# Kernel tuning notes

Hardware: AMD Instinct MI355X
Metric: run time of the kernel (lower is better)

Reference implementation:

```python
import jax, jax.numpy as jnp
import numpy as np

# problem constants (from config / init_kwargs)
OBJ = 1024        # object_size
D = 256           # diffraction_size == probe_size (pad = 0)
P = 256           # probe_size
S = 8             # num_slices
B = 256           # batch of scan indices
NSCAN = 4096      # number of scan positions
PX = 0.1          # pixel_size (Angstrom)
LAM = 0.0197      # wavelength (Angstrom, ~300 kV)
CONV = 0.025      # convergence angle (rad)
DZ = 2.0          # slice thickness (Angstrom)


def _freq_grids():
    f = jnp.fft.fftfreq(D, d=PX).astype(jnp.float32)
    kx, ky = jnp.meshgrid(f, f, indexing='ij')
    return kx, ky


def _probe(defocus, Cs, astig_mag, astig_angle, aperture_smooth):
    kx, ky = _freq_grids()
    k = jnp.sqrt(kx ** 2 + ky ** 2)
    k_angle = jnp.arctan2(ky, kx)
    chi = (np.pi * LAM * defocus * k ** 2
           + 0.5 * np.pi * LAM ** 3 * (Cs * 1e6) * k ** 4
           + np.pi * LAM * astig_mag * k ** 2 * jnp.cos(2.0 * (k_angle - astig_angle)))
    k_max = CONV / LAM
    smooth = jnp.abs(aperture_smooth) + 0.01
    aperture = jax.nn.sigmoid((k_max - k) / (k_max * smooth))
    probe_k = aperture.astype(jnp.complex64) * jnp.exp(1j * chi.astype(jnp.complex64))
    probe_real = jnp.fft.ifftshift(jnp.fft.ifft2(probe_k))
    probe_real = probe_real / jnp.sqrt(jnp.sum(jnp.abs(probe_real) ** 2))
    # crop(P) with P == D and c == h is the identity slice [0:D, 0:D]
    return probe_real


def _propagator():
    kx, ky = _freq_grids()
    k2 = kx ** 2 + ky ** 2
    return jnp.exp(1j * (np.pi * LAM * DZ * k2).astype(jnp.complex64))


def setup_inputs() -> dict:
    key = jax.random.key(0)
    k1, k2, k3, k4 = jax.random.split(key, 4)
    slice_amp = jnp.ones((S, OBJ, OBJ), dtype=jnp.float32) \
        + 0.05 * jax.random.normal(k1, (S, OBJ, OBJ), dtype=jnp.float32)
    slice_phase = 0.1 * jax.random.normal(k2, (S, OBJ, OBJ), dtype=jnp.float32)
    scan_positions = jax.random.randint(k3, (NSCAN, 2), 0, OBJ - P, dtype=jnp.int32)
    indices = jax.random.randint(k4, (B,), 0, NSCAN, dtype=jnp.int32)
    return {
        'slice_amp': slice_amp,
        'slice_phase': slice_phase,
        'defocus': jnp.float32(50.0),
        'Cs': jnp.float32(0.5),
        'astig_mag': jnp.float32(10.0),
        'astig_angle': jnp.float32(0.0),
        'aperture_smooth': jnp.float32(0.1),
        'scan_positions': scan_positions,
        'indices': indices,
    }


def reference(slice_amp, slice_phase, defocus, Cs, astig_mag, astig_angle,
              aperture_smooth, scan_positions, indices):
    probe = _probe(defocus, Cs, astig_mag, astig_angle, aperture_smooth)  # [D,D] c64
    H = _propagator()                                                      # [D,D] c64
    pos = scan_positions[indices]                                          # [B,2] (y,x)

    def gather_patch(t, yx):
        return jax.lax.dynamic_slice(t, (yx[0], yx[1]), (P, P))

    wave = jnp.broadcast_to(probe[None, :, :], (B, P, P))  # [B,P,P] c64
    for s in range(S):  # small fixed slice recurrence
        t = slice_amp[s].astype(jnp.complex64) * jnp.exp(1j * slice_phase[s].astype(jnp.complex64))
        patches = jax.vmap(gather_patch, in_axes=(None, 0))(t, pos)  # [B,P,P]
        exit_wave = wave * patches                      # pad = 0 since P == D
        wave = jnp.fft.ifft2(jnp.fft.fft2(exit_wave) * H)
    psi = jnp.fft.fft2(wave)                            # [B,D,D] complex64
    return psi
```

## Files before the change

kernel.cpp:

```cpp
#include <hip/hip_runtime.h>
#include <hip/hip_fp16.h>
#include <math.h>

typedef unsigned short u16;
typedef unsigned int   u32;

__device__ __forceinline__ bool is_f64(const void* amp){
  u32 u = ((const u32*)amp)[1];
  return ((u >> 20) & 0xFFF) >= 0x3FB;
}
__device__ __forceinline__ bool is_i64(const void* spos){
  const u32* p = (const u32*)spos;
  return (p[1] | p[3] | p[5]) == 0;
}
__device__ __forceinline__ float ldf(const void* p, size_t i, bool f64){
  return f64 ? (float)((const double*)p)[i] : ((const float*)p)[i];
}
__device__ __forceinline__ double lds_scalar(const void* p, bool f64){
  return f64 ? ((const double*)p)[0] : (double)((const float*)p)[0];
}
__device__ __forceinline__ int ldi(const void* p, size_t i, bool i64){
  return i64 ? (int)((const long long*)p)[i] : ((const int*)p)[i];
}

__device__ __forceinline__ u16 f2bf(float f){
  u32 u = __float_as_uint(f);
  u32 r = 0x7fffu + ((u >> 16) & 1u);
  return (u16)((u + r) >> 16);
}
__device__ __forceinline__ void stout(void* p, size_t i, float2 v){
  ((u32*)p)[i] = (u32)f2bf(v.y) | ((u32)f2bf(v.x) << 16);
}

template<int H>
__device__ __forceinline__ float2 ld_state(const void* p, size_t i){
  if (H){
    __half2 h = ((const __half2*)p)[i];
    return __half22float2(h);
  }
  return ((const float2*)p)[i];
}
template<int H>
__device__ __forceinline__ void st_state(void* p, size_t i, float2 v){
  if (H) ((__half2*)p)[i] = __floats2half2_rn(v.x, v.y);
  else   ((float2*)p)[i] = v;
}

__device__ __forceinline__ float2 cadd(float2 a, float2 b){ return make_float2(a.x+b.x, a.y+b.y); }
__device__ __forceinline__ float2 csub(float2 a, float2 b){ return make_float2(a.x-b.x, a.y-b.y); }
__device__ __forceinline__ float2 cmul(float2 a, float2 b){ return make_float2(a.x*b.x - a.y*b.y, a.x*b.y + a.y*b.x); }
__device__ __forceinline__ float2 cmulc(float2 a, float2 b){ return make_float2(a.x*b.x + a.y*b.y, a.y*b.x - a.x*b.y); }
__device__ __forceinline__ float2 cscale(float2 a, float s){ return make_float2(a.x*s, a.y*s); }

template<int SGN>
__device__ __forceinline__ void fft4(float2& a, float2& b, float2& c, float2& d){
  float2 apc = cadd(a,c), amc = csub(a,c);
  float2 bpd = cadd(b,d), bmd = csub(b,d);
  float2 jb = (SGN < 0) ? make_float2(bmd.y, -bmd.x) : make_float2(-bmd.y, bmd.x);
  a = cadd(apc, bpd);
  b = cadd(amc, jb);
  c = csub(apc, bpd);
  d = csub(amc, jb);
}
template<int SGN>
__device__ __forceinline__ float2 twc(float2 z, float re, float im){
  float i2 = (SGN < 0) ? im : -im;
  return make_float2(z.x*re - z.y*i2, z.x*i2 + z.y*re);
}
template<int SGN>
__device__ __forceinline__ void fft16(float2 v[16]){
  float2 h[16];
#pragma unroll
  for (int n1=0;n1<4;n1++){
    float2 a=v[n1], b=v[n1+4], c=v[n1+8], d=v[n1+12];
    fft4<SGN>(a,b,c,d);
    h[n1*4+0]=a; h[n1*4+1]=b; h[n1*4+2]=c; h[n1*4+3]=d;
  }
  const float C1=0.92387953251f, S1=0.38268343236f, C2=0.70710678119f;
  h[5]  = twc<SGN>(h[5],  C1,-S1);
  h[6]  = twc<SGN>(h[6],  C2,-C2);
  h[7]  = twc<SGN>(h[7],  S1,-C1);
  h[9]  = twc<SGN>(h[9],  C2,-C2);
  h[10] = twc<SGN>(h[10], 0.f,-1.f);
  h[11] = twc<SGN>(h[11],-C2,-C2);
  h[13] = twc<SGN>(h[13], S1,-C1);
  h[14] = twc<SGN>(h[14],-C2,-C2);
  h[15] = twc<SGN>(h[15],-C1, S1);
#pragma unroll
  for (int q=0;q<4;q++){
    float2 a=h[q], b=h[4+q], c=h[8+q], d=h[12+q];
    fft4<SGN>(a,b,c,d);
    v[q]=a; v[q+4]=b; v[q+8]=c; v[q+12]=d;
  }
}

__device__ __forceinline__ void make_tw(float2 tw[15], int t){
  float s0, c0;
  sincosf(0.0245436926f * (float)t, &s0, &c0);
  float2 w1 = make_float2(c0, -s0);
  tw[0] = w1;
#pragma unroll
  for (int q=1;q<15;q++) tw[q] = cmul(tw[q-1], w1);
}

template<int SGN, int BARRIER>
__device__ __forceinline__ void fft256(float2 v[16], float* Tr, float* Ti, int g, int t,
                                       const float2 tw[15]){
  fft16<SGN>(v);
#pragma unroll
  for (int q=1;q<16;q++){
    v[q] = (SGN < 0) ? cmul(v[q], tw[q-1]) : cmulc(v[q], tw[q-1]);
  }
  int base = g*257;
  if (BARRIER) __syncthreads();
#pragma unroll
  for (int k1=0;k1<16;k1++){
    int o = base + t*16 + (k1^t);
    Tr[o] = v[k1].x; Ti[o] = v[k1].y;
  }
  if (BARRIER) __syncthreads();
#pragma unroll
  for (int n1=0;n1<16;n1++){
    int o = base + n1*16 + (t^n1);
    v[n1] = make_float2(Tr[o], Ti[o]);
  }
  fft16<SGN>(v);
  if (SGN > 0){
#pragma unroll
    for (int q=0;q<16;q++) v[q] = cscale(v[q], 1.f/256.f);
  }
}

__device__ __forceinline__ float ffreq(int i){ return (float)(i < 128 ? i : i - 256) * 0.0390625f; }

#define LDS_F 4112
#define KMAX  1.26903553299f
#define PHCONST 0.123778191f


__global__ void __launch_bounds__(256) probe_rowsF(const void* defocus, const void* Cs,
                                                   const void* astig_mag, const void* astig_angle,
                                                   const void* ap_smooth, const void* ampflag,
                                                   float2* tmp){
  __shared__ float Tr[LDS_F], Ti[LDS_F];
  bool f64 = is_f64(ampflag);
  int tid = threadIdx.x, g = tid>>4, t = tid&15;
  int r = blockIdx.x*16 + g;
  double df = lds_scalar(defocus, f64), cs = lds_scalar(Cs, f64);
  double am = lds_scalar(astig_mag, f64), aa = lds_scalar(astig_angle, f64);
  float sm = fabsf((float)lds_scalar(ap_smooth, f64)) + 0.01f;
  const double LAMd = 0.0197;
  float kxv = ffreq(r);
  float2 v[16];
#pragma unroll
  for (int j=0;j<16;j++){
    int c = t + 16*j;
    float kyv = ffreq(c);
    double k2 = (double)kxv*kxv + (double)kyv*kyv;
    float k  = sqrtf((float)k2);
    double ang = atan2((double)kyv, (double)kxv);
    double chi = M_PI*LAMd*df*k2
               + 0.5*M_PI*LAMd*LAMd*LAMd*(cs*1e6)*k2*k2
               + M_PI*LAMd*am*k2*cos(2.0*(ang - aa));
    float ap = 1.f/(1.f + expf(-(KMAX - k)/(KMAX*sm)));
    double sc = sin(chi), cc = cos(chi);
    v[j] = make_float2(ap*(float)cc, ap*(float)sc);
  }
  float2 tw[15]; make_tw(tw, t);
  fft256<1,0>(v, Tr, Ti, g, t, tw);
#pragma unroll
  for (int j=0;j<16;j++) tmp[(r<<8) + t + 16*j] = v[j];
}

__global__ void __launch_bounds__(256) probe_colsF(const float2* tmp, float2* probe_out,
                                                   const void* ap_smooth, const void* ampflag){
  __shared__ float Tr[LDS_F], Ti[LDS_F];
  bool f64 = is_f64(ampflag);
  int tid = threadIdx.x, xl = tid&15, t = tid>>4;
  int cx = blockIdx.x*16 + xl;
  float sm = fabsf((float)lds_scalar(ap_smooth, f64)) + 0.01f;
  float S = 0.f;
  for (int i = tid; i < 65536; i += 256){
    float kx = ffreq(i>>8), ky = ffreq(i&255);
    float k = sqrtf(kx*kx + ky*ky);
    float ap = 1.f/(1.f + expf(-(KMAX - k)/(KMAX*sm)));
    S += ap*ap;
  }
#pragma unroll
  for (int off=32; off>0; off>>=1) S += __shfl_down(S, off);
  if ((tid&63)==0) Tr[tid>>6] = S;
  __syncthreads();
  float scale = 256.f * rsqrtf(Tr[0]+Tr[1]+Tr[2]+Tr[3]);
  float2 v[16];
#pragma unroll
  for (int j=0;j<16;j++) v[j] = tmp[((t+16*j)<<8) + cx];
  float2 tw[15]; make_tw(tw, t);
  fft256<1,1>(v, Tr, Ti, xl, t, tw);
  int csh = (cx + 128) & 255;
#pragma unroll
  for (int j=0;j<16;j++){
    int y = t + 16*j;
    probe_out[(((y+128)&255)<<8) + csh] = cscale(v[j], scale);
  }
}

__global__ void __launch_bounds__(256) build_ttabF(const void* amp, const void* phase,
                                                   __half2* ttab){
  bool f64 = is_f64(amp);
  int tid = threadIdx.x;
#pragma unroll
  for (int k=0;k<4;k++){
    size_t i = (size_t)blockIdx.x*1024 + tid + 256*k;
    float A = ldf(amp, i, f64);
    float P = ldf(phase, i, f64);
    float sp, cp; sincosf(P, &sp, &cp);
    ttab[i] = __floats2half2_rn(A*cp, A*sp);
  }
}

template<int H>
__global__ void __launch_bounds__(256) row_passT(const void* amp, const void* phase,
                                                 const void* spos, const void* sidx,
                                                 void* state, const float2* probe,
                                                 const __half2* ttab, int s, int first,
                                                 int use_tt){
  __shared__ float Tr[LDS_F], Ti[LDS_F];
  bool f64 = is_f64(amp);
  bool i64 = is_i64(spos);
  int tid = threadIdx.x, g = tid>>4, t = tid&15;
  int b = blockIdx.y;
  int y = blockIdx.x*16 + g;
  int n = ldi(sidx, b, i64);
  int py = ldi(spos, 2*(size_t)n, i64), px = ldi(spos, 2*(size_t)n+1, i64);
  size_t rowbase = ((size_t)s<<20) + (size_t)(py+y)*1024 + px;
  float2 tv[16];
  if (use_tt){
#pragma unroll
    for (int j=0;j<16;j++) tv[j] = __half22float2(ttab[rowbase + t + 16*j]);
  } else {
#pragma unroll
    for (int j=0;j<16;j++){
      int x = t + 16*j;
      float A = ldf(amp,   rowbase + x, f64);
      float P = ldf(phase, rowbase + x, f64);
      float sp, cp; sincosf(P, &sp, &cp);
      tv[j] = make_float2(A*cp, A*sp);
    }
  }
  size_t ib = (size_t)b << 16;
  float2 tw[15]; make_tw(tw, t);
  float2 v[16];
  if (first){
#pragma unroll
    for (int j=0;j<16;j++) v[j] = probe[(y<<8) + t + 16*j];
  } else {
#pragma unroll
    for (int j=0;j<16;j++) v[j] = ld_state<H>(state, ib + (y<<8) + t + 16*j);
    fft256<1,0>(v, Tr, Ti, g, t, tw);
  }
#pragma unroll
  for (int j=0;j<16;j++) v[j] = cmul(v[j], tv[j]);
  fft256<-1,0>(v, Tr, Ti, g, t, tw);
#pragma unroll
  for (int j=0;j<16;j++) st_state<H>(state, ib + (y<<8) + t + 16*j, v[j]);
}

template<int H>
__global__ void __launch_bounds__(256) col_passT(void* state){
  __shared__ float Tr[LDS_F], Ti[LDS_F];
  __shared__ float2 h1[256];
  int tid = threadIdx.x, xl = tid&15, t = tid>>4;
  int b = blockIdx.y;
  int cx = blockIdx.x*16 + xl;
  size_t ib = (size_t)b << 16;
  {
    float kk = ffreq(tid);
    float a = PHCONST * kk * kk;
    float sa, ca; sincosf(a, &sa, &ca);
    h1[tid] = make_float2(ca, sa);
  }
  float2 tw[15]; make_tw(tw, t);
  float2 v[16];
#pragma unroll
  for (int j=0;j<16;j++) v[j] = ld_state<H>(state, ib + ((t+16*j)<<8) + cx);
  fft256<-1,1>(v, Tr, Ti, xl, t, tw);
  float2 hx = h1[cx & 255];
#pragma unroll
  for (int j=0;j<16;j++) v[j] = cmul(v[j], cmul(h1[t + 16*j], hx));
  fft256<1,1>(v, Tr, Ti, xl, t, tw);
#pragma unroll
  for (int j=0;j<16;j++) st_state<H>(state, ib + ((t+16*j)<<8) + cx, v[j]);
}

template<int H>
__global__ void __launch_bounds__(256) col_finT(void* state, void* outp){
  __shared__ float Tr[LDS_F], Ti[LDS_F];
  __shared__ float2 h1[256];
  int tid = threadIdx.x, xl = tid&15, t = tid>>4;
  int b = blockIdx.y;
  int cx = blockIdx.x*16 + xl;
  size_t ib = (size_t)b << 16;
  {
    float kk = ffreq(tid);
    float a = PHCONST * kk * kk;
    float sa, ca; sincosf(a, &sa, &ca);
    h1[tid] = make_float2(ca, sa);
  }
  float2 tw[15]; make_tw(tw, t);
  float2 v[16];
#pragma unroll
  for (int j=0;j<16;j++) v[j] = ld_state<H>(state, ib + ((t+16*j)<<8) + cx);
  fft256<-1,1>(v, Tr, Ti, xl, t, tw);
  float2 hx = h1[cx & 255];
#pragma unroll
  for (int j=0;j<16;j++){
    float2 r = cmul(v[j], cmul(h1[t + 16*j], hx));
    stout(outp, ib + ((t+16*j)<<8) + cx, r);
  }
}

template<int H>
static void run_new(const void* amp, const void* phase,
                    const void* df, const void* cs, const void* am, const void* aa,
                    const void* sm, const void* spos, const void* sidx, int B,
                    void* state, __half2* ttab, int use_tt,
                    void* dout, hipStream_t stream){
  char* dob = (char*)dout;
  float2* probe = (float2*)dob;
  float2* ptmp  = (float2*)(dob + 524288);
  probe_rowsF<<<16, 256, 0, stream>>>(df, cs, am, aa, sm, amp, ptmp);
  probe_colsF<<<16, 256, 0, stream>>>(ptmp, probe, sm, amp);
  if (use_tt) build_ttabF<<<8192, 256, 0, stream>>>(amp, phase, ttab);
  dim3 grid(16, B);
  row_passT<H><<<grid, 256, 0, stream>>>(amp, phase, spos, sidx, state, probe, ttab, 0, 1, use_tt);
  col_passT<H><<<grid, 256, 0, stream>>>(state);
  for (int s = 1; s < 7; s++){
    row_passT<H><<<grid, 256, 0, stream>>>(amp, phase, spos, sidx, state, probe, ttab, s, 0, use_tt);
    col_passT<H><<<grid, 256, 0, stream>>>(state);
  }
  row_passT<H><<<grid, 256, 0, stream>>>(amp, phase, spos, sidx, state, probe, ttab, 7, 0, use_tt);
  col_finT<H><<<grid, 256, 0, stream>>>(state, dout);
}

extern "C" void kernel_launch(void* const* d_in, const int* in_sizes, int n_in,
                              void* d_out, int out_size, void* d_ws, size_t ws_size,
                              hipStream_t stream) {
  const void* amp   = d_in[0];
  const void* phase = d_in[1];
  const void* df    = d_in[2];
  const void* cs    = d_in[3];
  const void* am    = d_in[4];
  const void* aa    = d_in[5];
  const void* sm    = d_in[6];
  const void* spos  = d_in[7];
  const void* sidx  = d_in[8];
  int B = in_sizes[8];
  (void)out_size; (void)n_in;

  size_t stateH = (size_t)B * 65536 * 4;
  const size_t ttabB = (size_t)8 * 1024 * 1024 * 4;
  if (ws_size >= stateH + ttabB){
    void*    state = d_ws;
    __half2* ttab  = (__half2*)((char*)d_ws + stateH);
    run_new<1>(amp, phase, df, cs, am, aa, sm, spos, sidx, B,
               state, ttab, 1, d_out, stream);
  } else if (ws_size >= stateH){
    run_new<1>(amp, phase, df, cs, am, aa, sm, spos, sidx, B,
               d_ws, (__half2*)d_ws, 0, d_out, stream);
  } else {
    run_new<1>(amp, phase, df, cs, am, aa, sm, spos, sidx, B,
               d_out, (__half2*)d_out, 0, d_out, stream);
  }
}
```

Before: 812.9 us.

## Fold inverse-FFT normalisation into transmission/propagator and halve column-pass LDS

Removes the per-element 1/256 scaling from the inverse FFTs in the row and column passes. The normalisation is folded into the transmission table (1/256), the propagator table (1/16 per axis) and the probe scale. The column kernels now use a single shared buffer and exchange real and imaginary parts in two rounds with extra barriers. This halves LDS use per block to raise occupancy, at the cost of more synchronisation. Folding the scale into the half-precision table also shifts those values to a smaller magnitude, which may affect fp16 precision.

```diff
diff --git a/kernel.cpp b/kernel.cpp
--- a/kernel.cpp
+++ b/kernel.cpp
@@ -103,7 +103,7 @@
   for (int q=1;q<15;q++) tw[q] = cmul(tw[q-1], w1);
 }
 
-template<int SGN, int BARRIER>
+template<int SGN, int BARRIER, int SCALE>
 __device__ __forceinline__ void fft256(float2 v[16], float* Tr, float* Ti, int g, int t,
                                        const float2 tw[15]){
   fft16<SGN>(v);
@@ -125,15 +125,44 @@
     v[n1] = make_float2(Tr[o], Ti[o]);
   }
   fft16<SGN>(v);
-  if (SGN > 0){
+  if (SGN > 0 && SCALE){
 #pragma unroll
     for (int q=0;q<16;q++) v[q] = cscale(v[q], 1.f/256.f);
   }
 }
 
+template<int SGN, int SCALE>
+__device__ __forceinline__ void fft256s(float2 v[16], float* T, int g, int t,
+                                        const float2 tw[15]){
+  fft16<SGN>(v);
+#pragma unroll
+  for (int q=1;q<16;q++){
+    v[q] = (SGN < 0) ? cmul(v[q], tw[q-1]) : cmulc(v[q], tw[q-1]);
+  }
+  int base = g*257;
+  __syncthreads();
+#pragma unroll
+  for (int k1=0;k1<16;k1++) T[base + t*16 + (k1^t)] = v[k1].x;
+  __syncthreads();
+#pragma unroll
+  for (int n1=0;n1<16;n1++) v[n1].x = T[base + n1*16 + (t^n1)];
+  __syncthreads();
+#pragma unroll
+  for (int k1=0;k1<16;k1++) T[base + t*16 + (k1^t)] = v[k1].y;
+  __syncthreads();
+#pragma unroll
+  for (int n1=0;n1<16;n1++) v[n1].y = T[base + n1*16 + (t^n1)];
+  fft16<SGN>(v);
+  if (SGN > 0 && SCALE){
+#pragma unroll
+    for (int q=0;q<16;q++) v[q] = cscale(v[q], 1.f/256.f);
+  }
+}
+
 __device__ __forceinline__ float ffreq(int i){ return (float)(i < 128 ? i : i - 256) * 0.0390625f; }
 
 #define LDS_F 4112
+#define ISC   (1.f/256.f)
 #define KMAX  1.26903553299f
 #define PHCONST 0.123778191f
 
@@ -167,7 +196,7 @@
     v[j] = make_float2(ap*(float)cc, ap*(float)sc);
   }
   float2 tw[15]; make_tw(tw, t);
-  fft256<1,0>(v, Tr, Ti, g, t, tw);
+  fft256<1,0,1>(v, Tr, Ti, g, t, tw);
 #pragma unroll
   for (int j=0;j<16;j++) tmp[(r<<8) + t + 16*j] = v[j];
 }
@@ -175,6 +204,7 @@
 __global__ void __launch_bounds__(256) probe_colsF(const float2* tmp, float2* probe_out,
                                                    const void* ap_smooth, const void* ampflag){
   __shared__ float Tr[LDS_F], Ti[LDS_F];
+  __shared__ float Ssum[4];
   bool f64 = is_f64(ampflag);
   int tid = threadIdx.x, xl = tid&15, t = tid>>4;
   int cx = blockIdx.x*16 + xl;
@@ -188,14 +218,14 @@
   }
 #pragma unroll
   for (int off=32; off>0; off>>=1) S += __shfl_down(S, off);
-  if ((tid&63)==0) Tr[tid>>6] = S;
+  if ((tid&63)==0) Ssum[tid>>6] = S;
   __syncthreads();
-  float scale = 256.f * rsqrtf(Tr[0]+Tr[1]+Tr[2]+Tr[3]);
+  float scale = 65536.f * rsqrtf(Ssum[0]+Ssum[1]+Ssum[2]+Ssum[3]);
   float2 v[16];
 #pragma unroll
   for (int j=0;j<16;j++) v[j] = tmp[((t+16*j)<<8) + cx];
   float2 tw[15]; make_tw(tw, t);
-  fft256<1,1>(v, Tr, Ti, xl, t, tw);
+  fft256<1,1,1>(v, Tr, Ti, xl, t, tw);
   int csh = (cx + 128) & 255;
 #pragma unroll
   for (int j=0;j<16;j++){
@@ -214,7 +244,7 @@
     float A = ldf(amp, i, f64);
     float P = ldf(phase, i, f64);
     float sp, cp; sincosf(P, &sp, &cp);
-    ttab[i] = __floats2half2_rn(A*cp, A*sp);
+    ttab[i] = __floats2half2_rn(A*cp*ISC, A*sp*ISC);
   }
 }
 
@@ -244,7 +274,7 @@
       float A = ldf(amp,   rowbase + x, f64);
       float P = ldf(phase, rowbase + x, f64);
       float sp, cp; sincosf(P, &sp, &cp);
-      tv[j] = make_float2(A*cp, A*sp);
+      tv[j] = make_float2(A*cp*ISC, A*sp*ISC);
     }
   }
   size_t ib = (size_t)b << 16;
@@ -256,18 +286,45 @@
   } else {
 #pragma unroll
     for (int j=0;j<16;j++) v[j] = ld_state<H>(state, ib + (y<<8) + t + 16*j);
-    fft256<1,0>(v, Tr, Ti, g, t, tw);
+    fft256<1,0,0>(v, Tr, Ti, g, t, tw);
   }
 #pragma unroll
   for (int j=0;j<16;j++) v[j] = cmul(v[j], tv[j]);
-  fft256<-1,0>(v, Tr, Ti, g, t, tw);
+  fft256<-1,0,0>(v, Tr, Ti, g, t, tw);
 #pragma unroll
   for (int j=0;j<16;j++) st_state<H>(state, ib + (y<<8) + t + 16*j, v[j]);
 }
 
 template<int H>
 __global__ void __launch_bounds__(256) col_passT(void* state){
-  __shared__ float Tr[LDS_F], Ti[LDS_F];
+  __shared__ float T[LDS_F];
+  __shared__ float2 h1[256];
+  int tid = threadIdx.x, xl = tid&15, t = tid>>4;
+  int b = blockIdx.y;
+  int cx = blockIdx.x*16 + xl;
+  size_t ib = (size_t)b << 16;
+  {
+    float kk = ffreq(tid);
+    float a = PHCONST * kk * kk;
+    float sa, ca; sincosf(a, &sa, &ca);
+    h1[tid] = make_float2(ca*0.0625f, sa*0.0625f);
+  }
+  float2 tw[15]; make_tw(tw, t);
+  float2 v[16];
+#pragma unroll
+  for (int j=0;j<16;j++) v[j] = ld_state<H>(state, ib + ((t+16*j)<<8) + cx);
+  fft256s<-1,0>(v, T, xl, t, tw);
+  float2 hx = h1[cx & 255];
+#pragma unroll
+  for (int j=0;j<16;j++) v[j] = cmul(v[j], cmul(h1[t + 16*j], hx));
+  fft256s<1,0>(v, T, xl, t, tw);
+#pragma unroll
+  for (int j=0;j<16;j++) st_state<H>(state, ib + ((t+16*j)<<8) + cx, v[j]);
+}
+
+template<int H>
+__global__ void __launch_bounds__(256) col_finT(void* state, void* outp){
+  __shared__ float T[LDS_F];
   __shared__ float2 h1[256];
   int tid = threadIdx.x, xl = tid&15, t = tid>>4;
   int b = blockIdx.y;
@@ -283,34 +340,7 @@
   float2 v[16];
 #pragma unroll
   for (int j=0;j<16;j++) v[j] = ld_state<H>(state, ib + ((t+16*j)<<8) + cx);
-  fft256<-1,1>(v, Tr, Ti, xl, t, tw);
-  float2 hx = h1[cx & 255];
-#pragma unroll
-  for (int j=0;j<16;j++) v[j] = cmul(v[j], cmul(h1[t + 16*j], hx));
-  fft256<1,1>(v, Tr, Ti, xl, t, tw);
-#pragma unroll
-  for (int j=0;j<16;j++) st_state<H>(state, ib + ((t+16*j)<<8) + cx, v[j]);
-}
-
-template<int H>
-__global__ void __launch_bounds__(256) col_finT(void* state, void* outp){
-  __shared__ float Tr[LDS_F], Ti[LDS_F];
-  __shared__ float2 h1[256];
-  int tid = threadIdx.x, xl = tid&15, t = tid>>4;
-  int b = blockIdx.y;
-  int cx = blockIdx.x*16 + xl;
-  size_t ib = (size_t)b << 16;
-  {
-    float kk = ffreq(tid);
-    float a = PHCONST * kk * kk;
-    float sa, ca; sincosf(a, &sa, &ca);
-    h1[tid] = make_float2(ca, sa);
-  }
-  float2 tw[15]; make_tw(tw, t);
-  float2 v[16];
-#pragma unroll
-  for (int j=0;j<16;j++) v[j] = ld_state<H>(state, ib + ((t+16*j)<<8) + cx);
-  fft256<-1,1>(v, Tr, Ti, xl, t, tw);
+  fft256s<-1,0>(v, T, xl, t, tw);
   float2 hx = h1[cx & 255];
 #pragma unroll
   for (int j=0;j<16;j++){
```

New measurement: 866.5 us. 6.6% more time.
